# Optimization experiments

Measured on AMD Instinct MI355X. Metric: run time of the kernel, lower is better.

The kernel has to match this reference:

```python
import jax, jax.numpy as jnp
import numpy as np

N, IN_DIM, HID, LAT, E = 8192, 512, 256, 128, 262144


def gcn_conv(x, W, b, src, dst, n):
    # PyG-style GCNConv: linear transform, add self-loops, D^-1/2 A D^-1/2 aggregation, bias.
    h = x @ W                                                  # [n, out]
    loops = jnp.arange(n)
    s = jnp.concatenate([src, loops])
    d = jnp.concatenate([dst, loops])
    deg = jax.ops.segment_sum(jnp.ones(s.shape[0], x.dtype), d, num_segments=n)
    dinv = jnp.where(deg > 0, jax.lax.rsqrt(deg), jnp.zeros((), x.dtype))
    norm = dinv[s] * dinv[d]                                   # [E+n]
    out = jax.ops.segment_sum(h[s] * norm[:, None], d, num_segments=n)
    return out + b


def setup_inputs() -> dict:
    key = jax.random.key(0)
    ks = jax.random.split(key, 9)
    x = jax.random.normal(ks[0], (N, IN_DIM), dtype=jnp.float32)
    edge_index = jax.random.randint(ks[1], (2, E), 0, N, dtype=jnp.int64)
    eps = jax.random.normal(ks[2], (N, LAT), dtype=jnp.float32)
    # Glorot-ish scaled params
    W1 = jax.random.normal(ks[3], (IN_DIM, HID), dtype=jnp.float32) / np.sqrt(IN_DIM)
    b1 = jnp.zeros((HID,), jnp.float32)
    Wmu = jax.random.normal(ks[4], (HID, LAT), dtype=jnp.float32) / np.sqrt(HID)
    bmu = jnp.zeros((LAT,), jnp.float32)
    Wls = jax.random.normal(ks[5], (HID, LAT), dtype=jnp.float32) / np.sqrt(HID)
    bls = jnp.zeros((LAT,), jnp.float32)
    return {"x": x, "edge_index": edge_index, "eps": eps,
            "W1": W1, "b1": b1, "Wmu": Wmu, "bmu": bmu, "Wls": Wls, "bls": bls}


def reference(x, edge_index, eps, W1, b1, Wmu, bmu, Wls, bls):
    src, dst = edge_index[0], edge_index[1]
    n = x.shape[0]
    h = jax.nn.relu(gcn_conv(x, W1, b1, src, dst, n))          # [N, HID]
    mu = gcn_conv(h, Wmu, bmu, src, dst, n)                    # [N, LAT]
    logstd = gcn_conv(h, Wls, bls, src, dst, n)                # [N, LAT]
    z = eps * jnp.exp(logstd) + mu                             # reparametrize (training mode)
    adj_recon = jax.nn.sigmoid(z @ z.T)                        # [N, N]
    return adj_recon, mu, logstd
```

## Files before the change

### kernel.cpp

```cpp
#include <hip/hip_runtime.h>

#define N_NODES 8192
#define IN_DIM  512
#define HID     256
#define LAT     128
#define NEDGE   262144

typedef __attribute__((ext_vector_type(8))) short  bf16x8;
typedef __attribute__((ext_vector_type(4))) float  f32x4;
typedef unsigned short u16;
typedef __attribute__((ext_vector_type(4))) unsigned short u16x4;

static __device__ inline u16 f2bf(float f) {
    unsigned u = __float_as_uint(f);
    unsigned r = (u + 0x7fffu + ((u >> 16) & 1u)) >> 16;
    return (u16)r;
}
static __device__ inline float bf2f(u16 s) {
    return __uint_as_float(((unsigned)s) << 16);
}


__global__ __launch_bounds__(256) void count_kernel(const int* __restrict__ dst,
                                                    int* __restrict__ cnt) {
    int e = blockIdx.x * 256 + threadIdx.x;
    atomicAdd(&cnt[dst[e]], 1);
}

__global__ __launch_bounds__(256) void dinv_kernel(const int* __restrict__ cnt,
                                                   float* __restrict__ dinv) {
    int v = blockIdx.x * 256 + threadIdx.x;
    dinv[v] = rsqrtf((float)cnt[v] + 1.0f);
}

__global__ __launch_bounds__(256) void scan_kernel(const int* __restrict__ cnt,
                                                   int* __restrict__ rowptr,
                                                   int* __restrict__ cursor) {
    __shared__ int part[256];
    const int t = threadIdx.x;
    const int base = t * 32;
    int local[32];
    int s = 0;
#pragma unroll
    for (int i = 0; i < 32; ++i) { local[i] = s; s += cnt[base + i]; }
    part[t] = s;
    __syncthreads();
    for (int off = 1; off < 256; off <<= 1) {
        int v = 0;
        if (t >= off) v = part[t - off];
        __syncthreads();
        if (t >= off) part[t] += v;
        __syncthreads();
    }
    int pre = (t == 0) ? 0 : part[t - 1];
#pragma unroll
    for (int i = 0; i < 32; ++i) {
        int r = pre + local[i];
        rowptr[base + i] = r;
        cursor[base + i] = r;
    }
    if (t == 255) rowptr[8192] = part[255];
}

__global__ __launch_bounds__(256) void fill_kernel(const int* __restrict__ src,
                                                   const int* __restrict__ dst,
                                                   int* __restrict__ cursor,
                                                   int* __restrict__ ebuf) {
    int e = blockIdx.x * 256 + threadIdx.x;
    int pos = atomicAdd(&cursor[dst[e]], 1);
    ebuf[pos] = src[e];
}


__global__ __launch_bounds__(256) void convx_kernel(const float* __restrict__ X,
                                                    u16* __restrict__ xh,
                                                    u16* __restrict__ xl) {
    int t = blockIdx.x * 256 + threadIdx.x;
    f32x4 v = *(const f32x4*)(X + (size_t)t * 4);
    u16x4 h, l;
#pragma unroll
    for (int j = 0; j < 4; ++j) {
        h[j] = f2bf(v[j]);
        l[j] = f2bf(v[j] - bf2f(h[j]));
    }
    *(u16x4*)(xh + (size_t)t * 4) = h;
    *(u16x4*)(xl + (size_t)t * 4) = l;
}

__global__ __launch_bounds__(256) void convw_kernel(const float* __restrict__ W,
                                                    u16* __restrict__ th,
                                                    u16* __restrict__ tl,
                                                    int K, int N, int Kld, int roff) {
    int e = blockIdx.x * 256 + threadIdx.x;
    if (e >= K * N) return;
    int k = e / N, n = e - k * N;
    float f = W[e];
    u16 hi = f2bf(f);
    u16 lo = f2bf(f - bf2f(hi));
    size_t o = (size_t)(roff + n) * Kld + k;
    th[o] = hi;
    tl[o] = lo;
}

__global__ __launch_bounds__(256) void gemm_mfma(const u16* __restrict__ Ah,
                                                 const u16* __restrict__ Al,
                                                 const u16* __restrict__ Bth,
                                                 const u16* __restrict__ Btl,
                                                 float* __restrict__ C,
                                                 int K, int ldc) {
    const int lane = threadIdx.x & 63;
    const int wave = threadIdx.x >> 6;
    const int l16 = lane & 15, quad = lane >> 4;
    const int rowBase = blockIdx.y * 128 + (wave >> 1) * 64;
    const int colBase = blockIdx.x * 128 + (wave & 1) * 64;

    f32x4 acc[4][4] = {};

    for (int k0 = 0; k0 < K; k0 += 32) {
        const int kk = k0 + quad * 8;
        bf16x8 ah[4], al[4], bh[4], bl[4];
#pragma unroll
        for (int r = 0; r < 4; ++r) {
            int row = rowBase + r * 16 + l16;
            ah[r] = *(const bf16x8*)(Ah + (size_t)row * K + kk);
            al[r] = *(const bf16x8*)(Al + (size_t)row * K + kk);
        }
#pragma unroll
        for (int c = 0; c < 4; ++c) {
            int row = colBase + c * 16 + l16;
            bh[c] = *(const bf16x8*)(Bth + (size_t)row * K + kk);
            bl[c] = *(const bf16x8*)(Btl + (size_t)row * K + kk);
        }
#pragma unroll
        for (int r = 0; r < 4; ++r)
#pragma unroll
            for (int c = 0; c < 4; ++c) {
                acc[r][c] = __builtin_amdgcn_mfma_f32_16x16x32_bf16(ah[r], bh[c], acc[r][c], 0, 0, 0);
                acc[r][c] = __builtin_amdgcn_mfma_f32_16x16x32_bf16(ah[r], bl[c], acc[r][c], 0, 0, 0);
                acc[r][c] = __builtin_amdgcn_mfma_f32_16x16x32_bf16(al[r], bh[c], acc[r][c], 0, 0, 0);
            }
    }

#pragma unroll
    for (int r = 0; r < 4; ++r)
#pragma unroll
        for (int c = 0; c < 4; ++c)
#pragma unroll
            for (int i = 0; i < 4; ++i) {
                int orow = rowBase + r * 16 + quad * 4 + i;
                int ocol = colBase + c * 16 + l16;
                C[(size_t)orow * ldc + ocol] = acc[r][c][i];
            }
}

__global__ __launch_bounds__(256) void gather1_kernel(const float* __restrict__ pre1,
                                                      u16* __restrict__ h1h,
                                                      u16* __restrict__ h1l,
                                                      const int* __restrict__ rowptr,
                                                      const int* __restrict__ ebuf,
                                                      const float* __restrict__ dinv,
                                                      const float* __restrict__ b1) {
    const int wave = threadIdx.x >> 6, lane = threadIdx.x & 63;
    const int v = blockIdx.x * 4 + wave;
    const int c = lane * 4;
    const float dv = dinv[v];
    f32x4 acc = *(const f32x4*)(pre1 + (size_t)v * HID + c);
    acc *= dv * dv;
    int i = rowptr[v], end = rowptr[v + 1];
    for (; i + 1 < end; i += 2) {
        int s0 = ebuf[i], s1 = ebuf[i + 1];
        float n0 = dv * dinv[s0], n1 = dv * dinv[s1];
        f32x4 h0 = *(const f32x4*)(pre1 + (size_t)s0 * HID + c);
        f32x4 h1v = *(const f32x4*)(pre1 + (size_t)s1 * HID + c);
#pragma unroll
        for (int j = 0; j < 4; ++j) acc[j] += n0 * h0[j] + n1 * h1v[j];
    }
    if (i < end) {
        int s0 = ebuf[i];
        float n0 = dv * dinv[s0];
        f32x4 h0 = *(const f32x4*)(pre1 + (size_t)s0 * HID + c);
#pragma unroll
        for (int j = 0; j < 4; ++j) acc[j] += n0 * h0[j];
    }
    f32x4 bb = *(const f32x4*)(b1 + c);
    u16x4 hv, lv;
#pragma unroll
    for (int j = 0; j < 4; ++j) {
        float h = fmaxf(acc[j] + bb[j], 0.0f);
        hv[j] = f2bf(h);
        lv[j] = f2bf(h - bf2f(hv[j]));
    }
    *(u16x4*)(h1h + (size_t)v * HID + c) = hv;
    *(u16x4*)(h1l + (size_t)v * HID + c) = lv;
}

__global__ __launch_bounds__(256) void gather2_kernel(const float* __restrict__ pre2,
                                                      const int* __restrict__ rowptr,
                                                      const int* __restrict__ ebuf,
                                                      const float* __restrict__ dinv,
                                                      const float* __restrict__ bmu,
                                                      const float* __restrict__ bls,
                                                      const float* __restrict__ eps,
                                                      float* __restrict__ out_mu,
                                                      float* __restrict__ out_ls,
                                                      u16* __restrict__ zhi,
                                                      u16* __restrict__ zlo) {
    const int wave = threadIdx.x >> 6, lane = threadIdx.x & 63;
    const int v = blockIdx.x * 4 + wave;
    const int c = lane * 4;
    const float dv = dinv[v];
    f32x4 acc = *(const f32x4*)(pre2 + (size_t)v * HID + c);
    acc *= dv * dv;
    int i = rowptr[v], end = rowptr[v + 1];
    for (; i + 1 < end; i += 2) {
        int s0 = ebuf[i], s1 = ebuf[i + 1];
        float n0 = dv * dinv[s0], n1 = dv * dinv[s1];
        f32x4 h0 = *(const f32x4*)(pre2 + (size_t)s0 * HID + c);
        f32x4 h1v = *(const f32x4*)(pre2 + (size_t)s1 * HID + c);
#pragma unroll
        for (int j = 0; j < 4; ++j) acc[j] += n0 * h0[j] + n1 * h1v[j];
    }
    if (i < end) {
        int s0 = ebuf[i];
        float n0 = dv * dinv[s0];
        f32x4 h0 = *(const f32x4*)(pre2 + (size_t)s0 * HID + c);
#pragma unroll
        for (int j = 0; j < 4; ++j) acc[j] += n0 * h0[j];
    }
    const float* bias = (lane < 32) ? (bmu + c) : (bls + (c - 128));
    f32x4 bb = *(const f32x4*)bias;
#pragma unroll
    for (int j = 0; j < 4; ++j) acc[j] += bb[j];

    f32x4 other;
#pragma unroll
    for (int j = 0; j < 4; ++j) other[j] = __shfl(acc[j], (lane + 32) & 63, 64);

    if (lane < 32) {
        int idx = v * LAT + c;
        f32x4 ep = *(const f32x4*)(eps + idx);
        *(f32x4*)(out_mu + idx) = acc;
#pragma unroll
        for (int j = 0; j < 4; ++j) {
            float z = ep[j] * __expf(other[j]) + acc[j];
            u16 hi = f2bf(z);
            zhi[idx + j] = hi;
            zlo[idx + j] = f2bf(z - bf2f(hi));
        }
    } else {
        int idx = v * LAT + (c - 128);
        *(f32x4*)(out_ls + idx) = acc;
    }
}

__global__ __launch_bounds__(256) void zzt_kernel(const u16* __restrict__ zhi,
                                                  const u16* __restrict__ zlo,
                                                  float* __restrict__ out) {
    const int lane = threadIdx.x & 63;
    const int wave = threadIdx.x >> 6;
    const int l16 = lane & 15, quad = lane >> 4;
    const int rowBase = blockIdx.y * 128 + (wave >> 1) * 64;
    const int colBase = blockIdx.x * 128 + (wave & 1) * 64;

    f32x4 acc[4][4] = {};

#pragma unroll
    for (int k0 = 0; k0 < LAT; k0 += 32) {
        const int kk = k0 + quad * 8;
        bf16x8 ah[4], al[4], bh[4], bl[4];
#pragma unroll
        for (int r = 0; r < 4; ++r) {
            int row = rowBase + r * 16 + l16;
            ah[r] = *(const bf16x8*)(zhi + (size_t)row * LAT + kk);
            al[r] = *(const bf16x8*)(zlo + (size_t)row * LAT + kk);
        }
#pragma unroll
        for (int c = 0; c < 4; ++c) {
            int row = colBase + c * 16 + l16;
            bh[c] = *(const bf16x8*)(zhi + (size_t)row * LAT + kk);
            bl[c] = *(const bf16x8*)(zlo + (size_t)row * LAT + kk);
        }
#pragma unroll
        for (int r = 0; r < 4; ++r)
#pragma unroll
            for (int c = 0; c < 4; ++c) {
                acc[r][c] = __builtin_amdgcn_mfma_f32_16x16x32_bf16(ah[r], bh[c], acc[r][c], 0, 0, 0);
                acc[r][c] = __builtin_amdgcn_mfma_f32_16x16x32_bf16(ah[r], bl[c], acc[r][c], 0, 0, 0);
                acc[r][c] = __builtin_amdgcn_mfma_f32_16x16x32_bf16(al[r], bh[c], acc[r][c], 0, 0, 0);
            }
    }

#pragma unroll
    for (int r = 0; r < 4; ++r)
#pragma unroll
        for (int c = 0; c < 4; ++c)
#pragma unroll
            for (int i = 0; i < 4; ++i) {
                int orow = rowBase + r * 16 + quad * 4 + i;
                int ocol = colBase + c * 16 + l16;
                float t = acc[r][c][i];
                out[(size_t)orow * N_NODES + ocol] = 1.0f / (1.0f + __expf(-t));
            }
}

extern "C" void kernel_launch(void* const* d_in, const int* in_sizes, int n_in,
                              void* d_out, int out_size, void* d_ws, size_t ws_size,
                              hipStream_t stream) {
    const float* x   = (const float*)d_in[0];
    const int*   ei  = (const int*)d_in[1];
    const float* eps = (const float*)d_in[2];
    const float* W1  = (const float*)d_in[3];
    const float* b1  = (const float*)d_in[4];
    const float* Wmu = (const float*)d_in[5];
    const float* bmu = (const float*)d_in[6];
    const float* Wls = (const float*)d_in[7];
    const float* bls = (const float*)d_in[8];
    const int* src = ei;
    const int* dst = ei + NEDGE;

    float* out = (float*)d_out;
    float* pre1 = out;
    float* pre2 = out + 2097152;
    int*   ibase  = (int*)(out + 4194304);
    int*   cnt    = ibase;
    int*   rowptr = ibase + 8192;
    int*   cursor = ibase + 16385;
    int*   ebuf   = ibase + 24577;
    u16* xhi    = (u16*)(out + 4587520);
    u16* xlo    = (u16*)(out + 6684672);
    u16* h1hi   = (u16*)(out + 8781824);
    u16* h1lo   = (u16*)(out + 9830400);
    u16* w1thi  = (u16*)(out + 10878976);
    u16* w1tlo  = (u16*)(out + 11010048);
    u16* wcathi = (u16*)(out + 11141120);
    u16* wcatlo = (u16*)(out + 11173888);
    float* out_mu = out + 67108864;
    float* out_ls = out + 68157440;

    float* dinv = (float*)d_ws;
    u16* zhi = (u16*)((char*)d_ws + 32768);
    u16* zlo = (u16*)((char*)d_ws + 32768 + 2097152);

    hipMemsetAsync(cnt, 0, 8192 * sizeof(int), stream);

    count_kernel<<<NEDGE / 256, 256, 0, stream>>>(dst, cnt);
    dinv_kernel<<<N_NODES / 256, 256, 0, stream>>>(cnt, dinv);
    scan_kernel<<<1, 256, 0, stream>>>(cnt, rowptr, cursor);
    fill_kernel<<<NEDGE / 256, 256, 0, stream>>>(src, dst, cursor, ebuf);

    convx_kernel<<<4096, 256, 0, stream>>>(x, xhi, xlo);
    convw_kernel<<<(IN_DIM * HID) / 256, 256, 0, stream>>>(W1, w1thi, w1tlo, IN_DIM, HID, IN_DIM, 0);
    convw_kernel<<<(HID * LAT) / 256, 256, 0, stream>>>(Wmu, wcathi, wcatlo, HID, LAT, HID, 0);
    convw_kernel<<<(HID * LAT) / 256, 256, 0, stream>>>(Wls, wcathi, wcatlo, HID, LAT, HID, LAT);

    gemm_mfma<<<dim3(HID / 128, N_NODES / 128), 256, 0, stream>>>(xhi, xlo, w1thi, w1tlo,
                                                                  pre1, IN_DIM, HID);
    gather1_kernel<<<N_NODES / 4, 256, 0, stream>>>(pre1, h1hi, h1lo, rowptr, ebuf, dinv, b1);

    gemm_mfma<<<dim3(HID / 128, N_NODES / 128), 256, 0, stream>>>(h1hi, h1lo, wcathi, wcatlo,
                                                                  pre2, HID, HID);

    gather2_kernel<<<N_NODES / 4, 256, 0, stream>>>(pre2, rowptr, ebuf, dinv, bmu, bls, eps,
                                                    out_mu, out_ls, zhi, zlo);

    zzt_kernel<<<dim3(64, 64), 256, 0, stream>>>(zhi, zlo, out);
}
```

Measured before the change: 544.8 us.

## Exploit symmetry of z·zᵀ: compute lower-triangular tiles and mirror-store

The decoder GEMM launches only the 2080 lower-triangular 128x128 tiles and writes each off-diagonal tile twice, once directly and once transposed. This roughly halves the MFMA work and the operand loads. Output stores become nontemporal, and the transposed copy is written as 16-byte vectors. The z hi/lo bf16 stores in gather2 are vectorised to 4-wide. The output write traffic stays the same and is the dominant cost, and the transposed stores have a different access pattern.

```diff
diff --git a/kernel.cpp b/kernel.cpp
--- a/kernel.cpp
+++ b/kernel.cpp
@@ -239,28 +239,39 @@
     if (lane < 32) {
         int idx = v * LAT + c;
         f32x4 ep = *(const f32x4*)(eps + idx);
-        *(f32x4*)(out_mu + idx) = acc;
+        __builtin_nontemporal_store(acc, (f32x4*)(out_mu + idx));
+        u16x4 hv, lv;
 #pragma unroll
         for (int j = 0; j < 4; ++j) {
             float z = ep[j] * __expf(other[j]) + acc[j];
             u16 hi = f2bf(z);
-            zhi[idx + j] = hi;
-            zlo[idx + j] = f2bf(z - bf2f(hi));
-        }
+            hv[j] = hi;
+            lv[j] = f2bf(z - bf2f(hi));
+        }
+        *(u16x4*)(zhi + idx) = hv;
+        *(u16x4*)(zlo + idx) = lv;
     } else {
         int idx = v * LAT + (c - 128);
-        *(f32x4*)(out_ls + idx) = acc;
-    }
-}
-
+        __builtin_nontemporal_store(acc, (f32x4*)(out_ls + idx));
+    }
+}
+
+#define NTRI 2080
 __global__ __launch_bounds__(256) void zzt_kernel(const u16* __restrict__ zhi,
                                                   const u16* __restrict__ zlo,
                                                   float* __restrict__ out) {
     const int lane = threadIdx.x & 63;
     const int wave = threadIdx.x >> 6;
     const int l16 = lane & 15, quad = lane >> 4;
-    const int rowBase = blockIdx.y * 128 + (wave >> 1) * 64;
-    const int colBase = blockIdx.x * 128 + (wave & 1) * 64;
+
+    int bid = (blockIdx.x & 7) * 260 + (blockIdx.x >> 3);
+    int by = (int)((sqrtf(8.0f * (float)bid + 1.0f) - 1.0f) * 0.5f);
+    while ((by + 1) * (by + 2) / 2 <= bid) ++by;
+    while (by * (by + 1) / 2 > bid) --by;
+    const int bx = bid - by * (by + 1) / 2;
+
+    const int rowBase = by * 128 + (wave >> 1) * 64;
+    const int colBase = bx * 128 + (wave & 1) * 64;
 
     f32x4 acc[4][4] = {};
 
@@ -290,17 +301,27 @@
             }
     }
 
+    const bool offdiag = (by != bx);
 #pragma unroll
     for (int r = 0; r < 4; ++r)
 #pragma unroll
-        for (int c = 0; c < 4; ++c)
+        for (int c = 0; c < 4; ++c) {
+            f32x4 sig;
+#pragma unroll
+            for (int i = 0; i < 4; ++i)
+                sig[i] = 1.0f / (1.0f + __expf(-acc[r][c][i]));
 #pragma unroll
             for (int i = 0; i < 4; ++i) {
                 int orow = rowBase + r * 16 + quad * 4 + i;
                 int ocol = colBase + c * 16 + l16;
-                float t = acc[r][c][i];
-                out[(size_t)orow * N_NODES + ocol] = 1.0f / (1.0f + __expf(-t));
-            }
+                __builtin_nontemporal_store(sig[i], out + (size_t)orow * N_NODES + ocol);
+            }
+            if (offdiag) {
+                int trow = colBase + c * 16 + l16;
+                int tcol = rowBase + r * 16 + quad * 4;
+                __builtin_nontemporal_store(sig, (f32x4*)(out + (size_t)trow * N_NODES + tcol));
+            }
+        }
 }
 
 extern "C" void kernel_launch(void* const* d_in, const int* in_sizes, int n_in,
@@ -363,5 +384,5 @@
     gather2_kernel<<<N_NODES / 4, 256, 0, stream>>>(pre2, rowptr, ebuf, dinv, bmu, bls, eps,
                                                     out_mu, out_ls, zhi, zlo);
 
-    zzt_kernel<<<dim3(64, 64), 256, 0, stream>>>(zhi, zlo, out);
-}
+    zzt_kernel<<<NTRI, 256, 0, stream>>>(zhi, zlo, out);
+}
```

Result: faster. 526.2 us (-3.4%).
